# Kernel optimization log

Hardware: AMD Instinct MI355X
Metric: run time of the kernel (lower is better)

Reference implementation:

```python
import jax, jax.numpy as jnp
import numpy as np

B, H, S, D = 2, 16, 2048, 64


def setup_inputs() -> dict:
    key = jax.random.key(0)
    kq, kk, kv, km = jax.random.split(key, 4)
    q = jax.random.normal(kq, (B, H, S, D), dtype=jnp.float32)
    k = jax.random.normal(kk, (B, H, S, D), dtype=jnp.float32)
    v = jax.random.normal(kv, (B, H, S, D), dtype=jnp.float32)
    # True = attend, False = masked out (padding)
    attention_mask = jax.random.randint(km, (B, S), 0, 2).astype(jnp.bool_)
    return {"q": q, "k": k, "v": v, "attention_mask": attention_mask}


def reference(q, k, v, attention_mask):
    scale = q.shape[-1] ** -0.5
    # sim: [B, H, S, S]
    sim = jnp.einsum("bhid,bhjd->bhij", q, k) * scale
    neg = jnp.finfo(sim.dtype).min
    # mask [B, S] -> [B, 1, 1, S]; keep where mask is True
    sim = jnp.where(attention_mask[:, None, None, :], sim, neg)
    attn = jax.nn.softmax(sim, axis=-1)
    out = jnp.einsum("bhij,bhjd->bhid", attn, v)
    return out
```

## Files before the change

kernel.cpp:

```cpp
#include <hip/hip_runtime.h>
#include <hip/hip_fp16.h>

namespace {
constexpr int kB = 2, kH = 16, kS = 2048, kD = 64, kBH = kB * kH;
constexpr int BQ = 128, BKV = 64;
constexpr int NQT = kS / BQ;

typedef _Float16 f16x8 __attribute__((ext_vector_type(8)));
typedef _Float16 f16x4 __attribute__((ext_vector_type(4)));
typedef __fp16 fp16x2 __attribute__((ext_vector_type(2)));
typedef float f32x16 __attribute__((ext_vector_type(16)));
typedef float f32x4 __attribute__((ext_vector_type(4)));
typedef unsigned int u32;

constexpr float kQScale = 0.125f * 1.4426950408889634f;

__device__ __forceinline__ int paddr(int row, int col) {
  const int prow = row >> 1;
  return prow * 128 + ((((row & 1) << 6) | col) ^ ((prow & 15) << 3));
}

__device__ __forceinline__ u32 pkrtz(float a, float b) {
  union { fp16x2 h; u32 u; } c;
  c.h = __builtin_amdgcn_cvt_pkrtz(a, b);
  return c.u;
}

__global__ __launch_bounds__(256) void scan_kernel(const int* __restrict__ M,
                                                   int* __restrict__ Idx,
                                                   float* __restrict__ BiasC,
                                                   int* __restrict__ NTarr) {
  const int b = blockIdx.x;
  const int tid = threadIdx.x;
  __shared__ int part[256];
  __shared__ int nvs;
  int m[8], sum = 0;
#pragma unroll
  for (int i = 0; i < 8; ++i) {
    m[i] = M[b * kS + tid * 8 + i];
    sum += m[i] ? 1 : 0;
  }
  part[tid] = sum;
  __syncthreads();
  for (int off = 1; off < 256; off <<= 1) {
    int v = (tid >= off) ? part[tid - off] : 0;
    __syncthreads();
    part[tid] += v;
    __syncthreads();
  }
  int run = part[tid] - sum;
#pragma unroll
  for (int i = 0; i < 8; ++i)
    if (m[i]) Idx[b * kS + run++] = tid * 8 + i;
  if (tid == 255) nvs = part[255];
  __syncthreads();
  const int Nv = nvs;
  int NT = (Nv + 63) >> 6;
  if (NT == 0) NT = 1;
  const int pad = NT * 64;
  for (int j = Nv + tid; j < pad; j += 256) Idx[b * kS + j] = 0;
#pragma unroll
  for (int i = 0; i < 8; ++i) {
    const int j = tid * 8 + i;
    BiasC[b * kS + j] = (j < Nv) ? 0.f : -1e30f;
  }
  if (tid == 0) NTarr[b] = NT;
}

__global__ __launch_bounds__(256) void gather_k_kernel(
    const float* __restrict__ K, const int* __restrict__ Idx,
    const int* __restrict__ NTarr, _Float16* __restrict__ Kc) {
  const int e = blockIdx.x * 256 + threadIdx.x;
  const int bh = e >> 14;
  const int rem = e & 16383;
  const int j = rem >> 3;
  const int d0 = (rem & 7) << 3;
  const int b = bh >> 4;
  if (j >= NTarr[b] * 64) return;
  const int src = Idx[b * kS + j];
  const float* p = K + ((size_t)bh * kS + src) * kD + d0;
  float4 x = *(const float4*)p;
  float4 y = *(const float4*)(p + 4);
  f16x8 o;
  o[0] = (_Float16)x.x; o[1] = (_Float16)x.y; o[2] = (_Float16)x.z; o[3] = (_Float16)x.w;
  o[4] = (_Float16)y.x; o[5] = (_Float16)y.y; o[6] = (_Float16)y.z; o[7] = (_Float16)y.w;
  *(f16x8*)(Kc + ((size_t)bh * kS + j) * kD + d0) = o;
}

__global__ __launch_bounds__(256) void gather_vt_kernel(
    const float* __restrict__ V, const int* __restrict__ Idx,
    const int* __restrict__ NTarr, _Float16* __restrict__ Vtc) {
  __shared__ _Float16 Vl[64 * 68];
  __shared__ int ridx[64];
  const int tid = threadIdx.x;
  const int bh = blockIdx.x >> 5;
  const int jt = blockIdx.x & 31;
  const int b = bh >> 4;
  if (jt >= NTarr[b]) return;
  if (tid < 64) ridx[tid] = Idx[b * kS + jt * 64 + tid];
  __syncthreads();
  const float* vb = V + (size_t)bh * kS * kD;
#pragma unroll
  for (int i = 0; i < 4; ++i) {
    int off = (tid + 256 * i) * 4;
    int r = off >> 6, c = off & 63;
    float4 x = *(const float4*)(vb + (size_t)ridx[r] * kD + c);
    Vl[(c + 0) * 68 + r] = (_Float16)x.x;
    Vl[(c + 1) * 68 + r] = (_Float16)x.y;
    Vl[(c + 2) * 68 + r] = (_Float16)x.z;
    Vl[(c + 3) * 68 + r] = (_Float16)x.w;
  }
  __syncthreads();
  const int d = tid >> 2, c0 = (tid & 3) * 16;
  _Float16* op = Vtc + ((size_t)bh * kD + d) * kS + jt * 64 + c0;
#pragma unroll
  for (int j = 0; j < 4; ++j)
    *(f16x4*)(op + 4 * j) = *(const f16x4*)(Vl + d * 68 + c0 + 4 * j);
}

__global__ __launch_bounds__(256, 2) void fattn_c(
    const _Float16* __restrict__ Kc, const _Float16* __restrict__ Vtc,
    const float* __restrict__ Q, const float* __restrict__ BiasC,
    const int* __restrict__ NTarr, float* __restrict__ O) {
  __shared__ __align__(16) char smem[16384 + 16384 + 512];
  _Float16* Kl = (_Float16*)smem;
  _Float16* Vl = (_Float16*)(smem + 16384);
  float* mbl = (float*)(smem + 32768);
  float* Os = (float*)smem;

  const int tid = threadIdx.x;
  const int lane = tid & 63;
  const int w = tid >> 6;
  const int q = lane & 31;
  const int h = lane >> 5;

  const int bid = blockIdx.x;
  const int cpx = gridDim.x >> 3;
  const int sbid = (bid & 7) * cpx + (bid >> 3);
  const int bh = sbid >> 4;
  const int qt = sbid & 15;
  const int q0 = qt * BQ;
  const int b = bh >> 4;
  const int NT = NTarr[b];

  f16x8 qf[4];
  {
    const float* qp = Q + ((size_t)bh * kS + q0 + w * 32 + q) * kD;
#pragma unroll
    for (int dc = 0; dc < 4; ++dc) {
      const float* p = qp + dc * 16 + h * 8;
      float4 x = *(const float4*)p;
      float4 y = *(const float4*)(p + 4);
      f16x8 a;
      a[0] = (_Float16)(x.x * kQScale); a[1] = (_Float16)(x.y * kQScale);
      a[2] = (_Float16)(x.z * kQScale); a[3] = (_Float16)(x.w * kQScale);
      a[4] = (_Float16)(y.x * kQScale); a[5] = (_Float16)(y.y * kQScale);
      a[6] = (_Float16)(y.z * kQScale); a[7] = (_Float16)(y.w * kQScale);
      qf[dc] = a;
    }
  }

  f32x16 oa[2];
#pragma unroll
  for (int i = 0; i < 16; ++i) { oa[0][i] = 0.f; oa[1][i] = 0.f; }
  float m_run = -30.f, l_run = 0.f;

  const _Float16* kb = Kc + (size_t)bh * kS * kD;
  const _Float16* vb = Vtc + (size_t)bh * kD * kS;
  const float* mpc = BiasC + b * kS;

  const int sr = tid >> 2, sc = (tid & 3) * 16;
  const int a0 = paddr(sr, sc), a1 = paddr(sr, sc + 8);

  {
    f16x8 k0 = *(const f16x8*)(kb + (size_t)sr * kD + sc);
    f16x8 k1 = *(const f16x8*)(kb + (size_t)sr * kD + sc + 8);
    f16x8 v0 = *(const f16x8*)(vb + (size_t)sr * kS + sc);
    f16x8 v1 = *(const f16x8*)(vb + (size_t)sr * kS + sc + 8);
    *(f16x8*)(Kl + a0) = k0; *(f16x8*)(Kl + a1) = k1;
    *(f16x8*)(Vl + a0) = v0; *(f16x8*)(Vl + a1) = v1;
    if (tid < 64) mbl[tid] = mpc[tid];
  }
  __syncthreads();

  int cur = 0;
  for (int t = 0; t < NT; ++t) {
    const int t0 = t * BKV;
    const bool pf = (t + 1 < NT);
    f16x8 nk0, nk1, nv0, nv1;
    float nmv = 0.f;
    if (pf) {
      const int n0 = t0 + BKV;
      nk0 = *(const f16x8*)(kb + (size_t)(n0 + sr) * kD + sc);
      nk1 = *(const f16x8*)(kb + (size_t)(n0 + sr) * kD + sc + 8);
      nv0 = *(const f16x8*)(vb + (size_t)sr * kS + n0 + sc);
      nv1 = *(const f16x8*)(vb + (size_t)sr * kS + n0 + sc + 8);
      if (tid < 64) nmv = mpc[n0 + tid];
    }

    const _Float16* kd = Kl + cur * 4096;
    const _Float16* vd = Vl + cur * 4096;
    const float* mb = mbl + cur * 64;

    f32x16 s[2];
    __builtin_amdgcn_s_setprio(1);
#pragma unroll
    for (int mt = 0; mt < 2; ++mt) {
      f32x16 z;
#pragma unroll
      for (int g = 0; g < 4; ++g) {
        f32x4 mv = *(const f32x4*)(mb + mt * 32 + 8 * g + 4 * h);
        z[4 * g + 0] = mv[0]; z[4 * g + 1] = mv[1];
        z[4 * g + 2] = mv[2]; z[4 * g + 3] = mv[3];
      }
#pragma unroll
      for (int dc = 0; dc < 4; ++dc) {
        f16x8 kf = *(const f16x8*)(kd + paddr(mt * 32 + q, dc * 16 + h * 8));
        z = __builtin_amdgcn_mfma_f32_32x32x16_f16(kf, qf[dc], z, 0, 0, 0);
      }
      s[mt] = z;
    }
    __builtin_amdgcn_s_setprio(0);

    float mx = -3.0e38f;
#pragma unroll
    for (int mt = 0; mt < 2; ++mt)
#pragma unroll
      for (int r = 0; r < 16; r += 2)
        mx = fmaxf(fmaxf(mx, s[mt][r]), s[mt][r + 1]);
    mx = fmaxf(mx, __shfl_xor(mx, 32));

    if (__any(mx > m_run + 8.f)) {
      const float mnew = fmaxf(m_run, mx);
      const float corr = __builtin_amdgcn_exp2f(m_run - mnew);
      m_run = mnew;
      l_run *= corr;
#pragma unroll
      for (int mt = 0; mt < 2; ++mt)
#pragma unroll
        for (int r = 0; r < 16; ++r) oa[mt][r] *= corr;
    }
    const float negm = -m_run;

    float ts = 0.f;
#pragma unroll
    for (int mt = 0; mt < 2; ++mt)
#pragma unroll
      for (int r = 0; r < 16; ++r) {
        float p = __builtin_amdgcn_exp2f(s[mt][r] + negm);
        s[mt][r] = p;
        ts += p;
      }
    ts += __shfl_xor(ts, 32);
    l_run += ts;

    u32 pkA[2][4], pkB[2][4];
#pragma unroll
    for (int mt = 0; mt < 2; ++mt)
#pragma unroll
      for (int g = 0; g < 4; ++g) {
        pkA[mt][g] = pkrtz(s[mt][4 * g + 0], s[mt][4 * g + 1]);
        pkB[mt][g] = pkrtz(s[mt][4 * g + 2], s[mt][4 * g + 3]);
      }

    __builtin_amdgcn_s_setprio(1);
#pragma unroll
    for (int kk = 0; kk < 4; ++kk) {
      const int e = kk & 1, mt = kk >> 1;
      u32 crossA = __shfl_xor(h ? pkA[mt][2 * e] : pkA[mt][2 * e + 1], 32);
      u32 crossB = __shfl_xor(h ? pkB[mt][2 * e] : pkB[mt][2 * e + 1], 32);
      union { u32 u[4]; f16x8 v; } pb;
      pb.u[0] = h ? crossA : pkA[mt][2 * e];
      pb.u[1] = h ? crossB : pkB[mt][2 * e];
      pb.u[2] = h ? pkA[mt][2 * e + 1] : crossA;
      pb.u[3] = h ? pkB[mt][2 * e + 1] : crossB;
#pragma unroll
      for (int md = 0; md < 2; ++md) {
        f16x8 vf = *(const f16x8*)(vd + paddr(md * 32 + q, kk * 16 + h * 8));
        oa[md] = __builtin_amdgcn_mfma_f32_32x32x16_f16(vf, pb.v, oa[md], 0, 0, 0);
      }
    }
    __builtin_amdgcn_s_setprio(0);

    if (pf) {
      _Float16* kd2 = Kl + (cur ^ 1) * 4096;
      _Float16* vd2 = Vl + (cur ^ 1) * 4096;
      *(f16x8*)(kd2 + a0) = nk0; *(f16x8*)(kd2 + a1) = nk1;
      *(f16x8*)(vd2 + a0) = nv0; *(f16x8*)(vd2 + a1) = nv1;
      if (tid < 64) mbl[(cur ^ 1) * 64 + tid] = nmv;
    }
    __syncthreads();
    cur ^= 1;
  }

  const float inv = 1.f / l_run;
#pragma unroll
  for (int ph = 0; ph < 2; ++ph) {
    __syncthreads();
    if ((w >> 1) == ph) {
#pragma unroll
      for (int mt = 0; mt < 2; ++mt)
#pragma unroll
        for (int r = 0; r < 16; ++r) {
          int d = mt * 32 + (r & 3) + 8 * (r >> 2) + 4 * h;
          Os[((w & 1) * 32 + q) * 68 + d] = oa[mt][r] * inv;
        }
    }
    __syncthreads();
    {
      const int row = tid >> 2, cb = (tid & 3) * 16;
      float* op = O + ((size_t)bh * kS + q0 + ph * 64 + row) * kD + cb;
      const float* sp = Os + row * 68 + cb;
#pragma unroll
      for (int j = 0; j < 4; ++j) *(float4*)(op + 4 * j) = *(const float4*)(sp + 4 * j);
    }
  }
}

__device__ __forceinline__ int swz(int row, int colh) {
  return row * 64 + (colh ^ ((row & 7) << 3));
}

__global__ __launch_bounds__(256, 4) void fattn_fallback(
    const float* __restrict__ Q, const float* __restrict__ K,
    const float* __restrict__ V, const int* __restrict__ M,
    float* __restrict__ O) {
  __shared__ __align__(16) _Float16 Kl[64 * 64];
  __shared__ __align__(16) _Float16 Vtl[64 * 64];
  __shared__ __align__(16) _Float16 Pl[64 * 64];
  __shared__ float mbl[64];

  const int tid = threadIdx.x;
  const int lane = tid & 63;
  const int w = tid >> 6;
  const int lr = lane & 15;
  const int hg = lane >> 4;
  const int NQT1 = kS / 64;
  const int bh = blockIdx.x / NQT1;
  const int qt = blockIdx.x % NQT1;
  const int b = bh / kH;
  const int q0 = qt * 64;

  f16x8 aq[2];
  {
    const int row = q0 + w * 16 + lr;
    const float* qp = Q + ((size_t)bh * kS + row) * kD;
#pragma unroll
    for (int kf = 0; kf < 2; ++kf) {
      const float* p = qp + kf * 32 + hg * 8;
      float4 x = *(const float4*)(p);
      float4 y = *(const float4*)(p + 4);
      f16x8 a;
      a[0] = (_Float16)(x.x * 0.125f); a[1] = (_Float16)(x.y * 0.125f);
      a[2] = (_Float16)(x.z * 0.125f); a[3] = (_Float16)(x.w * 0.125f);
      a[4] = (_Float16)(y.x * 0.125f); a[5] = (_Float16)(y.y * 0.125f);
      a[6] = (_Float16)(y.z * 0.125f); a[7] = (_Float16)(y.w * 0.125f);
      aq[kf] = a;
    }
  }

  f32x4 oacc[4];
#pragma unroll
  for (int c = 0; c < 4; ++c) { oacc[c][0]=0.f; oacc[c][1]=0.f; oacc[c][2]=0.f; oacc[c][3]=0.f; }
  float m_run[4], l_run[4];
#pragma unroll
  for (int r = 0; r < 4; ++r) { m_run[r] = -1e30f; l_run[r] = 0.f; }

  const float* kb = K + (size_t)bh * kS * kD;
  const float* vb = V + (size_t)bh * kS * kD;
  const int* mbp = M + b * kS;

  for (int t0 = 0; t0 < kS; t0 += 64) {
    __syncthreads();
#pragma unroll
    for (int i = 0; i < 4; ++i) {
      const int off = (tid + 256 * i) * 4;
      const int row = off >> 6;
      const int col = off & 63;
      float4 kx = *(const float4*)(kb + (size_t)(t0 + row) * kD + col);
      f16x4 hk;
      hk[0] = (_Float16)kx.x; hk[1] = (_Float16)kx.y;
      hk[2] = (_Float16)kx.z; hk[3] = (_Float16)kx.w;
      *(f16x4*)(Kl + swz(row, col)) = hk;
      float4 vx = *(const float4*)(vb + (size_t)(t0 + row) * kD + col);
      Vtl[swz(col + 0, row)] = (_Float16)vx.x;
      Vtl[swz(col + 1, row)] = (_Float16)vx.y;
      Vtl[swz(col + 2, row)] = (_Float16)vx.z;
      Vtl[swz(col + 3, row)] = (_Float16)vx.w;
    }
    if (tid < 64) mbl[tid] = mbp[t0 + tid] ? 0.f : -1e30f;
    __syncthreads();

    f32x4 s[4];
#pragma unroll
    for (int c = 0; c < 4; ++c) {
      f32x4 z; z[0]=0.f; z[1]=0.f; z[2]=0.f; z[3]=0.f;
#pragma unroll
      for (int kf = 0; kf < 2; ++kf) {
        f16x8 bk = *(const f16x8*)(Kl + swz(c * 16 + lr, kf * 32 + hg * 8));
        z = __builtin_amdgcn_mfma_f32_16x16x32_f16(aq[kf], bk, z, 0, 0, 0);
      }
      const float mval = mbl[c * 16 + lr];
#pragma unroll
      for (int r = 0; r < 4; ++r) z[r] += mval;
      s[c] = z;
    }

    float tmax[4];
#pragma unroll
    for (int r = 0; r < 4; ++r)
      tmax[r] = fmaxf(fmaxf(s[0][r], s[1][r]), fmaxf(s[2][r], s[3][r]));
#pragma unroll
    for (int off = 1; off < 16; off <<= 1)
#pragma unroll
      for (int r = 0; r < 4; ++r) tmax[r] = fmaxf(tmax[r], __shfl_xor(tmax[r], off));

    float mnew[4], corr[4], tsum[4];
#pragma unroll
    for (int r = 0; r < 4; ++r) {
      mnew[r] = fmaxf(m_run[r], tmax[r]);
      corr[r] = __expf(m_run[r] - mnew[r]);
      m_run[r] = mnew[r];
      tsum[r] = 0.f;
    }
#pragma unroll
    for (int c = 0; c < 4; ++c)
#pragma unroll
      for (int r = 0; r < 4; ++r) {
        const float p = __expf(s[c][r] - mnew[r]);
        tsum[r] += p;
        Pl[swz(w * 16 + hg * 4 + r, c * 16 + lr)] = (_Float16)p;
      }
#pragma unroll
    for (int off = 1; off < 16; off <<= 1)
#pragma unroll
      for (int r = 0; r < 4; ++r) tsum[r] += __shfl_xor(tsum[r], off);
#pragma unroll
    for (int r = 0; r < 4; ++r) l_run[r] = l_run[r] * corr[r] + tsum[r];
#pragma unroll
    for (int c = 0; c < 4; ++c)
#pragma unroll
      for (int r = 0; r < 4; ++r) oacc[c][r] *= corr[r];

#pragma unroll
    for (int kf = 0; kf < 2; ++kf) {
      f16x8 pa = *(const f16x8*)(Pl + swz(w * 16 + lr, kf * 32 + hg * 8));
#pragma unroll
      for (int cd = 0; cd < 4; ++cd) {
        f16x8 vbf = *(const f16x8*)(Vtl + swz(cd * 16 + lr, kf * 32 + hg * 8));
        oacc[cd] = __builtin_amdgcn_mfma_f32_16x16x32_f16(pa, vbf, oacc[cd], 0, 0, 0);
      }
    }
  }

#pragma unroll
  for (int r = 0; r < 4; ++r) {
    const float inv = 1.f / l_run[r];
    const int row = q0 + w * 16 + hg * 4 + r;
    float* op = O + ((size_t)bh * kS + row) * kD;
#pragma unroll
    for (int cd = 0; cd < 4; ++cd) op[cd * 16 + lr] = oacc[cd][r] * inv;
  }
}
}

extern "C" void kernel_launch(void* const* d_in, const int* in_sizes, int n_in,
                              void* d_out, int out_size, void* d_ws, size_t ws_size,
                              hipStream_t stream) {
  (void)in_sizes; (void)n_in; (void)out_size;
  const float* q = (const float*)d_in[0];
  const float* k = (const float*)d_in[1];
  const float* v = (const float*)d_in[2];
  const int* m = (const int*)d_in[3];
  float* o = (float*)d_out;

  const size_t elems = (size_t)kBH * kS * kD;
  const size_t need = 2 * elems * sizeof(_Float16)
                    + (size_t)kB * kS * sizeof(int)
                    + (size_t)kB * kS * sizeof(float)
                    + 256;

  if (ws_size >= need) {
    _Float16* Kc = (_Float16*)d_ws;
    _Float16* Vtc = Kc + elems;
    int* Idx = (int*)(Vtc + elems);
    float* BiasC = (float*)(Idx + (size_t)kB * kS);
    int* NTarr = (int*)(BiasC + (size_t)kB * kS);
    hipLaunchKernelGGL(scan_kernel, dim3(kB), dim3(256), 0, stream, m, Idx, BiasC, NTarr);
    hipLaunchKernelGGL(gather_k_kernel, dim3((kBH * kS * 8) / 256), dim3(256), 0, stream,
                       k, Idx, NTarr, Kc);
    hipLaunchKernelGGL(gather_vt_kernel, dim3(kBH * (kS / 64)), dim3(256), 0, stream,
                       v, Idx, NTarr, Vtc);
    hipLaunchKernelGGL(fattn_c, dim3(kBH * NQT), dim3(256), 0, stream,
                       Kc, Vtc, q, BiasC, NTarr, o);
  } else {
    hipLaunchKernelGGL(fattn_fallback, dim3(kBH * (kS / 64)), dim3(256), 0, stream,
                       q, k, v, m, o);
  }
}
```

Measured before the change: 54.57 us.

## Load K/V fragments directly from global into registers, dropping LDS staging

The attention kernel no longer stages K and V tiles through double-buffered shared memory with block-wide barriers. Each wave now loads its MFMA operand fragments straight from global memory (L2-cached) into registers, prefetching the next K tile and ping-ponging two register buffers. The mask bias is read from global too. Row max and sum reductions become tree reductions to shorten dependency chains. This removes LDS traffic and __syncthreads per tile, at the cost of each of the four waves reading the same K/V from global/L2 again and higher register pressure.

```diff
diff --git a/kernel.cpp b/kernel.cpp
--- a/kernel.cpp
+++ b/kernel.cpp
@@ -14,11 +14,6 @@
 typedef unsigned int u32;
 
 constexpr float kQScale = 0.125f * 1.4426950408889634f;
-
-__device__ __forceinline__ int paddr(int row, int col) {
-  const int prow = row >> 1;
-  return prow * 128 + ((((row & 1) << 6) | col) ^ ((prow & 15) << 3));
-}
 
 __device__ __forceinline__ u32 pkrtz(float a, float b) {
   union { fp16x2 h; u32 u; } c;
@@ -118,15 +113,11 @@
     *(f16x4*)(op + 4 * j) = *(const f16x4*)(Vl + d * 68 + c0 + 4 * j);
 }
 
-__global__ __launch_bounds__(256, 2) void fattn_c(
+__global__ __launch_bounds__(256, 2) void fattn_d(
     const _Float16* __restrict__ Kc, const _Float16* __restrict__ Vtc,
     const float* __restrict__ Q, const float* __restrict__ BiasC,
     const int* __restrict__ NTarr, float* __restrict__ O) {
-  __shared__ __align__(16) char smem[16384 + 16384 + 512];
-  _Float16* Kl = (_Float16*)smem;
-  _Float16* Vl = (_Float16*)(smem + 16384);
-  float* mbl = (float*)(smem + 32768);
-  float* Os = (float*)smem;
+  __shared__ float Os[64 * 68];
 
   const int tid = threadIdx.x;
   const int lane = tid & 63;
@@ -169,39 +160,34 @@
   const _Float16* vb = Vtc + (size_t)bh * kD * kS;
   const float* mpc = BiasC + b * kS;
 
-  const int sr = tid >> 2, sc = (tid & 3) * 16;
-  const int a0 = paddr(sr, sc), a1 = paddr(sr, sc + 8);
-
-  {
-    f16x8 k0 = *(const f16x8*)(kb + (size_t)sr * kD + sc);
-    f16x8 k1 = *(const f16x8*)(kb + (size_t)sr * kD + sc + 8);
-    f16x8 v0 = *(const f16x8*)(vb + (size_t)sr * kS + sc);
-    f16x8 v1 = *(const f16x8*)(vb + (size_t)sr * kS + sc + 8);
-    *(f16x8*)(Kl + a0) = k0; *(f16x8*)(Kl + a1) = k1;
-    *(f16x8*)(Vl + a0) = v0; *(f16x8*)(Vl + a1) = v1;
-    if (tid < 64) mbl[tid] = mpc[tid];
-  }
-  __syncthreads();
-
-  int cur = 0;
-  for (int t = 0; t < NT; ++t) {
-    const int t0 = t * BKV;
-    const bool pf = (t + 1 < NT);
-    f16x8 nk0, nk1, nv0, nv1;
-    float nmv = 0.f;
-    if (pf) {
-      const int n0 = t0 + BKV;
-      nk0 = *(const f16x8*)(kb + (size_t)(n0 + sr) * kD + sc);
-      nk1 = *(const f16x8*)(kb + (size_t)(n0 + sr) * kD + sc + 8);
-      nv0 = *(const f16x8*)(vb + (size_t)sr * kS + n0 + sc);
-      nv1 = *(const f16x8*)(vb + (size_t)sr * kS + n0 + sc + 8);
-      if (tid < 64) nmv = mpc[n0 + tid];
-    }
-
-    const _Float16* kd = Kl + cur * 4096;
-    const _Float16* vd = Vl + cur * 4096;
-    const float* mb = mbl + cur * 64;
-
+  const _Float16* kbase0 = kb + (q + 0) * 64 + h * 8;
+  const _Float16* kbase1 = kb + (q + 32) * 64 + h * 8;
+  const _Float16* vbase0 = vb + (size_t)(q + 0) * kS + h * 8;
+  const _Float16* vbase1 = vb + (size_t)(q + 32) * kS + h * 8;
+
+  f16x8 kA[8], kB[8], vr[8];
+  auto loadK = [&](int t, f16x8 (&kr)[8]) {
+    const int off = t * 4096;
+#pragma unroll
+    for (int dc = 0; dc < 4; ++dc) {
+      kr[dc] = *(const f16x8*)(kbase0 + off + dc * 16);
+      kr[4 + dc] = *(const f16x8*)(kbase1 + off + dc * 16);
+    }
+  };
+  auto loadV = [&](int t) {
+    const int off = t * 64;
+#pragma unroll
+    for (int kk = 0; kk < 4; ++kk) {
+      vr[kk] = *(const f16x8*)(vbase0 + off + kk * 16);
+      vr[4 + kk] = *(const f16x8*)(vbase1 + off + kk * 16);
+    }
+  };
+
+  auto body = [&](int t, f16x8 (&kcur)[8], f16x8 (&knext)[8], bool pf) {
+    loadV(t);
+    if (pf) loadK(t + 1, knext);
+
+    const float* mb = mpc + t * 64;
     f32x16 s[2];
     __builtin_amdgcn_s_setprio(1);
 #pragma unroll
@@ -214,21 +200,20 @@
         z[4 * g + 2] = mv[2]; z[4 * g + 3] = mv[3];
       }
 #pragma unroll
-      for (int dc = 0; dc < 4; ++dc) {
-        f16x8 kf = *(const f16x8*)(kd + paddr(mt * 32 + q, dc * 16 + h * 8));
-        z = __builtin_amdgcn_mfma_f32_32x32x16_f16(kf, qf[dc], z, 0, 0, 0);
-      }
+      for (int dc = 0; dc < 4; ++dc)
+        z = __builtin_amdgcn_mfma_f32_32x32x16_f16(kcur[mt * 4 + dc], qf[dc], z, 0, 0, 0);
       s[mt] = z;
     }
     __builtin_amdgcn_s_setprio(0);
 
-    float mx = -3.0e38f;
-#pragma unroll
-    for (int mt = 0; mt < 2; ++mt)
-#pragma unroll
-      for (int r = 0; r < 16; r += 2)
-        mx = fmaxf(fmaxf(mx, s[mt][r]), s[mt][r + 1]);
-    mx = fmaxf(mx, __shfl_xor(mx, 32));
+    float tm[16];
+#pragma unroll
+    for (int i = 0; i < 16; ++i) tm[i] = fmaxf(s[0][i], s[1][i]);
+#pragma unroll
+    for (int st = 8; st > 0; st >>= 1)
+#pragma unroll
+      for (int i = 0; i < st; ++i) tm[i] = fmaxf(tm[i], tm[i + st]);
+    const float mx = fmaxf(tm[0], __shfl_xor(tm[0], 32));
 
     if (__any(mx > m_run + 8.f)) {
       const float mnew = fmaxf(m_run, mx);
@@ -242,56 +227,55 @@
     }
     const float negm = -m_run;
 
-    float ts = 0.f;
 #pragma unroll
     for (int mt = 0; mt < 2; ++mt)
 #pragma unroll
-      for (int r = 0; r < 16; ++r) {
-        float p = __builtin_amdgcn_exp2f(s[mt][r] + negm);
-        s[mt][r] = p;
-        ts += p;
-      }
-    ts += __shfl_xor(ts, 32);
-    l_run += ts;
-
-    u32 pkA[2][4], pkB[2][4];
+      for (int r = 0; r < 16; ++r)
+        s[mt][r] = __builtin_amdgcn_exp2f(s[mt][r] + negm);
+    float tsum[16];
+#pragma unroll
+    for (int i = 0; i < 16; ++i) tsum[i] = s[0][i] + s[1][i];
+#pragma unroll
+    for (int st = 8; st > 0; st >>= 1)
+#pragma unroll
+      for (int i = 0; i < st; ++i) tsum[i] += tsum[i + st];
+    l_run += tsum[0] + __shfl_xor(tsum[0], 32);
+
+    u32 pkA_[2][4], pkB_[2][4];
 #pragma unroll
     for (int mt = 0; mt < 2; ++mt)
 #pragma unroll
       for (int g = 0; g < 4; ++g) {
-        pkA[mt][g] = pkrtz(s[mt][4 * g + 0], s[mt][4 * g + 1]);
-        pkB[mt][g] = pkrtz(s[mt][4 * g + 2], s[mt][4 * g + 3]);
+        pkA_[mt][g] = pkrtz(s[mt][4 * g + 0], s[mt][4 * g + 1]);
+        pkB_[mt][g] = pkrtz(s[mt][4 * g + 2], s[mt][4 * g + 3]);
       }
 
     __builtin_amdgcn_s_setprio(1);
 #pragma unroll
     for (int kk = 0; kk < 4; ++kk) {
       const int e = kk & 1, mt = kk >> 1;
-      u32 crossA = __shfl_xor(h ? pkA[mt][2 * e] : pkA[mt][2 * e + 1], 32);
-      u32 crossB = __shfl_xor(h ? pkB[mt][2 * e] : pkB[mt][2 * e + 1], 32);
+      u32 crossA = __shfl_xor(h ? pkA_[mt][2 * e] : pkA_[mt][2 * e + 1], 32);
+      u32 crossB = __shfl_xor(h ? pkB_[mt][2 * e] : pkB_[mt][2 * e + 1], 32);
       union { u32 u[4]; f16x8 v; } pb;
-      pb.u[0] = h ? crossA : pkA[mt][2 * e];
-      pb.u[1] = h ? crossB : pkB[mt][2 * e];
-      pb.u[2] = h ? pkA[mt][2 * e + 1] : crossA;
-      pb.u[3] = h ? pkB[mt][2 * e + 1] : crossB;
-#pragma unroll
-      for (int md = 0; md < 2; ++md) {
-        f16x8 vf = *(const f16x8*)(vd + paddr(md * 32 + q, kk * 16 + h * 8));
-        oa[md] = __builtin_amdgcn_mfma_f32_32x32x16_f16(vf, pb.v, oa[md], 0, 0, 0);
-      }
+      pb.u[0] = h ? crossA : pkA_[mt][2 * e];
+      pb.u[1] = h ? crossB : pkB_[mt][2 * e];
+      pb.u[2] = h ? pkA_[mt][2 * e + 1] : crossA;
+      pb.u[3] = h ? pkB_[mt][2 * e + 1] : crossB;
+#pragma unroll
+      for (int md = 0; md < 2; ++md)
+        oa[md] = __builtin_amdgcn_mfma_f32_32x32x16_f16(vr[md * 4 + kk], pb.v, oa[md], 0, 0, 0);
     }
     __builtin_amdgcn_s_setprio(0);
-
-    if (pf) {
-      _Float16* kd2 = Kl + (cur ^ 1) * 4096;
-      _Float16* vd2 = Vl + (cur ^ 1) * 4096;
-      *(f16x8*)(kd2 + a0) = nk0; *(f16x8*)(kd2 + a1) = nk1;
-      *(f16x8*)(vd2 + a0) = nv0; *(f16x8*)(vd2 + a1) = nv1;
-      if (tid < 64) mbl[(cur ^ 1) * 64 + tid] = nmv;
-    }
-    __syncthreads();
-    cur ^= 1;
-  }
+  };
+
+  loadK(0, kA);
+  int t = 0;
+  while (t + 2 <= NT) {
+    body(t, kA, kB, true);
+    body(t + 1, kB, kA, t + 2 < NT);
+    t += 2;
+  }
+  if (t < NT) body(t, kA, kB, false);
 
   const float inv = 1.f / l_run;
 #pragma unroll
@@ -491,7 +475,7 @@
                        k, Idx, NTarr, Kc);
     hipLaunchKernelGGL(gather_vt_kernel, dim3(kBH * (kS / 64)), dim3(256), 0, stream,
                        v, Idx, NTarr, Vtc);
-    hipLaunchKernelGGL(fattn_c, dim3(kBH * NQT), dim3(256), 0, stream,
+    hipLaunchKernelGGL(fattn_d, dim3(kBH * NQT), dim3(256), 0, stream,
                        Kc, Vtc, q, BiasC, NTarr, o);
   } else {
     hipLaunchKernelGGL(fattn_fallback, dim3(kBH * (kS / 64)), dim3(256), 0, stream,
```

After: 97.26 us. 78.2% more time.

## Split KV range across two wavegroups per block with in-block softmax merge

Applied to the files above, without the earlier changes.

Halves the query tile to 64 rows and doubles the grid. Each block's two 128-thread halves now process separate halves of the compacted KV tiles, each with its own double-buffered LDS, and their partial (m, l, O) states are merged through shared memory at the end. NT is padded to an even count so the split is balanced. The max and sum reductions are also rewritten as trees to shorten the dependency chains. The goal is more parallelism and shorter per-block serial KV loops, at the cost of 65KB of LDS per block (which may limit occupancy), a merge epilogue, and K/V being reloaded by twice as many blocks.

```diff
diff --git a/kernel.cpp b/kernel.cpp
--- a/kernel.cpp
+++ b/kernel.cpp
@@ -3,7 +3,7 @@
 
 namespace {
 constexpr int kB = 2, kH = 16, kS = 2048, kD = 64, kBH = kB * kH;
-constexpr int BQ = 128, BKV = 64;
+constexpr int BQ = 64, BKV = 64;
 constexpr int NQT = kS / BQ;
 
 typedef _Float16 f16x8 __attribute__((ext_vector_type(8)));
@@ -57,6 +57,7 @@
   const int Nv = nvs;
   int NT = (Nv + 63) >> 6;
   if (NT == 0) NT = 1;
+  NT += (NT & 1);
   const int pad = NT * 64;
   for (int j = Nv + tid; j < pad; j += 256) Idx[b * kS + j] = 0;
 #pragma unroll
@@ -118,34 +119,37 @@
     *(f16x4*)(op + 4 * j) = *(const f16x4*)(Vl + d * 68 + c0 + 4 * j);
 }
 
-__global__ __launch_bounds__(256, 2) void fattn_c(
+__global__ __launch_bounds__(256, 2) void fattn_m(
     const _Float16* __restrict__ Kc, const _Float16* __restrict__ Vtc,
     const float* __restrict__ Q, const float* __restrict__ BiasC,
     const int* __restrict__ NTarr, float* __restrict__ O) {
-  __shared__ __align__(16) char smem[16384 + 16384 + 512];
-  _Float16* Kl = (_Float16*)smem;
-  _Float16* Vl = (_Float16*)(smem + 16384);
-  float* mbl = (float*)(smem + 32768);
-  float* Os = (float*)smem;
+  __shared__ __align__(16) char smem[66560];
 
   const int tid = threadIdx.x;
   const int lane = tid & 63;
-  const int w = tid >> 6;
   const int q = lane & 31;
   const int h = lane >> 5;
+  const int pr = tid >> 7;
+  const int pw = (tid >> 6) & 1;
 
   const int bid = blockIdx.x;
   const int cpx = gridDim.x >> 3;
   const int sbid = (bid & 7) * cpx + (bid >> 3);
-  const int bh = sbid >> 4;
-  const int qt = sbid & 15;
+  const int bh = sbid >> 5;
+  const int qt = sbid & 31;
   const int q0 = qt * BQ;
   const int b = bh >> 4;
   const int NT = NTarr[b];
+  const int NTh = NT >> 1;
+  const int g0 = pr * NTh;
+
+  _Float16* Kl = (_Float16*)(smem + pr * 32768);
+  _Float16* Vl = (_Float16*)(smem + pr * 32768 + 16384);
+  float* mbl = (float*)(smem + 65536 + pr * 512);
 
   f16x8 qf[4];
   {
-    const float* qp = Q + ((size_t)bh * kS + q0 + w * 32 + q) * kD;
+    const float* qp = Q + ((size_t)bh * kS + q0 + pw * 32 + q) * kD;
 #pragma unroll
     for (int dc = 0; dc < 4; ++dc) {
       const float* p = qp + dc * 16 + h * 8;
@@ -169,34 +173,43 @@
   const _Float16* vb = Vtc + (size_t)bh * kD * kS;
   const float* mpc = BiasC + b * kS;
 
-  const int sr = tid >> 2, sc = (tid & 3) * 16;
-  const int a0 = paddr(sr, sc), a1 = paddr(sr, sc + 8);
-
-  {
-    f16x8 k0 = *(const f16x8*)(kb + (size_t)sr * kD + sc);
-    f16x8 k1 = *(const f16x8*)(kb + (size_t)sr * kD + sc + 8);
-    f16x8 v0 = *(const f16x8*)(vb + (size_t)sr * kS + sc);
-    f16x8 v1 = *(const f16x8*)(vb + (size_t)sr * kS + sc + 8);
-    *(f16x8*)(Kl + a0) = k0; *(f16x8*)(Kl + a1) = k1;
-    *(f16x8*)(Vl + a0) = v0; *(f16x8*)(Vl + a1) = v1;
-    if (tid < 64) mbl[tid] = mpc[tid];
-  }
+  const int ptid = tid & 127;
+  const int sr = ptid >> 1, scb = (ptid & 1) * 32;
+  int adr[4];
+#pragma unroll
+  for (int c = 0; c < 4; ++c) adr[c] = paddr(sr, scb + 8 * c);
+
+  f16x8 nk[4], nv[4];
+  float nmb = 0.f;
+  auto loadT = [&](int g) {
+    const _Float16* kp = kb + (size_t)(g * 64 + sr) * kD + scb;
+    const _Float16* vp = vb + (size_t)sr * kS + g * 64 + scb;
+#pragma unroll
+    for (int c = 0; c < 4; ++c) {
+      nk[c] = *(const f16x8*)(kp + 8 * c);
+      nv[c] = *(const f16x8*)(vp + 8 * c);
+    }
+    if (ptid < 64) nmb = mpc[g * 64 + ptid];
+  };
+  auto writeT = [&](int buf) {
+    _Float16* kd = Kl + buf * 4096;
+    _Float16* vd = Vl + buf * 4096;
+#pragma unroll
+    for (int c = 0; c < 4; ++c) {
+      *(f16x8*)(kd + adr[c]) = nk[c];
+      *(f16x8*)(vd + adr[c]) = nv[c];
+    }
+    if (ptid < 64) mbl[buf * 64 + ptid] = nmb;
+  };
+
+  loadT(g0);
+  writeT(0);
   __syncthreads();
 
   int cur = 0;
-  for (int t = 0; t < NT; ++t) {
-    const int t0 = t * BKV;
-    const bool pf = (t + 1 < NT);
-    f16x8 nk0, nk1, nv0, nv1;
-    float nmv = 0.f;
-    if (pf) {
-      const int n0 = t0 + BKV;
-      nk0 = *(const f16x8*)(kb + (size_t)(n0 + sr) * kD + sc);
-      nk1 = *(const f16x8*)(kb + (size_t)(n0 + sr) * kD + sc + 8);
-      nv0 = *(const f16x8*)(vb + (size_t)sr * kS + n0 + sc);
-      nv1 = *(const f16x8*)(vb + (size_t)sr * kS + n0 + sc + 8);
-      if (tid < 64) nmv = mpc[n0 + tid];
-    }
+  for (int i = 0; i < NTh; ++i) {
+    const bool pf = (i + 1 < NTh);
+    if (pf) loadT(g0 + i + 1);
 
     const _Float16* kd = Kl + cur * 4096;
     const _Float16* vd = Vl + cur * 4096;
@@ -222,13 +235,14 @@
     }
     __builtin_amdgcn_s_setprio(0);
 
-    float mx = -3.0e38f;
-#pragma unroll
-    for (int mt = 0; mt < 2; ++mt)
-#pragma unroll
-      for (int r = 0; r < 16; r += 2)
-        mx = fmaxf(fmaxf(mx, s[mt][r]), s[mt][r + 1]);
-    mx = fmaxf(mx, __shfl_xor(mx, 32));
+    float tm[16];
+#pragma unroll
+    for (int i2 = 0; i2 < 16; ++i2) tm[i2] = fmaxf(s[0][i2], s[1][i2]);
+#pragma unroll
+    for (int st = 8; st > 0; st >>= 1)
+#pragma unroll
+      for (int i2 = 0; i2 < st; ++i2) tm[i2] = fmaxf(tm[i2], tm[i2 + st]);
+    const float mx = fmaxf(tm[0], __shfl_xor(tm[0], 32));
 
     if (__any(mx > m_run + 8.f)) {
       const float mnew = fmaxf(m_run, mx);
@@ -242,17 +256,19 @@
     }
     const float negm = -m_run;
 
-    float ts = 0.f;
 #pragma unroll
     for (int mt = 0; mt < 2; ++mt)
 #pragma unroll
-      for (int r = 0; r < 16; ++r) {
-        float p = __builtin_amdgcn_exp2f(s[mt][r] + negm);
-        s[mt][r] = p;
-        ts += p;
-      }
-    ts += __shfl_xor(ts, 32);
-    l_run += ts;
+      for (int r = 0; r < 16; ++r)
+        s[mt][r] = __builtin_amdgcn_exp2f(s[mt][r] + negm);
+    float tsum[16];
+#pragma unroll
+    for (int i2 = 0; i2 < 16; ++i2) tsum[i2] = s[0][i2] + s[1][i2];
+#pragma unroll
+    for (int st = 8; st > 0; st >>= 1)
+#pragma unroll
+      for (int i2 = 0; i2 < st; ++i2) tsum[i2] += tsum[i2 + st];
+    l_run += tsum[0] + __shfl_xor(tsum[0], 32);
 
     u32 pkA[2][4], pkB[2][4];
 #pragma unroll
@@ -282,38 +298,46 @@
     }
     __builtin_amdgcn_s_setprio(0);
 
-    if (pf) {
-      _Float16* kd2 = Kl + (cur ^ 1) * 4096;
-      _Float16* vd2 = Vl + (cur ^ 1) * 4096;
-      *(f16x8*)(kd2 + a0) = nk0; *(f16x8*)(kd2 + a1) = nk1;
-      *(f16x8*)(vd2 + a0) = nv0; *(f16x8*)(vd2 + a1) = nv1;
-      if (tid < 64) mbl[(cur ^ 1) * 64 + tid] = nmv;
-    }
+    if (pf) writeT(cur ^ 1);
     __syncthreads();
     cur ^= 1;
   }
 
-  const float inv = 1.f / l_run;
-#pragma unroll
-  for (int ph = 0; ph < 2; ++ph) {
-    __syncthreads();
-    if ((w >> 1) == ph) {
-#pragma unroll
-      for (int mt = 0; mt < 2; ++mt)
-#pragma unroll
-        for (int r = 0; r < 16; ++r) {
-          int d = mt * 32 + (r & 3) + 8 * (r >> 2) + 4 * h;
-          Os[((w & 1) * 32 + q) * 68 + d] = oa[mt][r] * inv;
-        }
-    }
-    __syncthreads();
-    {
-      const int row = tid >> 2, cb = (tid & 3) * 16;
-      float* op = O + ((size_t)bh * kS + q0 + ph * 64 + row) * kD + cb;
-      const float* sp = Os + row * 68 + cb;
-#pragma unroll
-      for (int j = 0; j < 4; ++j) *(float4*)(op + 4 * j) = *(const float4*)(sp + 4 * j);
-    }
+  float* O1 = (float*)(smem + 32768);
+  float* ml1 = (float*)(smem + 49152);
+  if (pr == 1) {
+#pragma unroll
+    for (int mt = 0; mt < 2; ++mt)
+#pragma unroll
+      for (int r = 0; r < 16; ++r)
+        O1[(mt * 16 + r) * 128 + (pw * 32 + q) * 2 + h] = oa[mt][r];
+    if (h == 0) *(float2*)(ml1 + (pw * 32 + q) * 2) = make_float2(m_run, l_run);
+  }
+  __syncthreads();
+  float* Os = (float*)smem;
+  if (pr == 0) {
+    const float2 m1l1 = *(const float2*)(ml1 + (pw * 32 + q) * 2);
+    const float mm = fmaxf(m_run, m1l1.x);
+    float w0 = __builtin_amdgcn_exp2f(m_run - mm);
+    float w1 = __builtin_amdgcn_exp2f(m1l1.x - mm);
+    const float inv = 1.f / (l_run * w0 + m1l1.y * w1);
+    w0 *= inv; w1 *= inv;
+#pragma unroll
+    for (int mt = 0; mt < 2; ++mt)
+#pragma unroll
+      for (int r = 0; r < 16; ++r) {
+        const int d = mt * 32 + (r & 3) + 8 * (r >> 2) + 4 * h;
+        const float v1 = O1[(mt * 16 + r) * 128 + (pw * 32 + q) * 2 + h];
+        Os[(pw * 32 + q) * 68 + d] = oa[mt][r] * w0 + v1 * w1;
+      }
+  }
+  __syncthreads();
+  {
+    const int row = tid >> 2, cb = (tid & 3) * 16;
+    float* op = O + ((size_t)bh * kS + q0 + row) * kD + cb;
+    const float* sp = Os + row * 68 + cb;
+#pragma unroll
+    for (int j = 0; j < 4; ++j) *(float4*)(op + 4 * j) = *(const float4*)(sp + 4 * j);
   }
 }
 
@@ -491,7 +515,7 @@
                        k, Idx, NTarr, Kc);
     hipLaunchKernelGGL(gather_vt_kernel, dim3(kBH * (kS / 64)), dim3(256), 0, stream,
                        v, Idx, NTarr, Vtc);
-    hipLaunchKernelGGL(fattn_c, dim3(kBH * NQT), dim3(256), 0, stream,
+    hipLaunchKernelGGL(fattn_m, dim3(kBH * NQT), dim3(256), 0, stream,
                        Kc, Vtc, q, BiasC, NTarr, o);
   } else {
     hipLaunchKernelGGL(fattn_fallback, dim3(kBH * (kS / 64)), dim3(256), 0, stream,
```

After: 63.05 us. +15.5%, slower.

## Fuse K and V gather kernels and replace bias buffer with tail masking

Applied to the files above, without the earlier changes.

Merges the separate K-gather and V-transpose-gather kernels into one launch that shares the loaded row indices, dropping one kernel launch. Removes the per-key bias array: the attention kernel now starts MFMA accumulators at zero and masks only the padded keys of the final tile by comparing against the valid-key count. Max and sum reductions become tree reductions to shorten dependency chains. This trades LDS bias loads and stores per tile for a branch on the last tile.

```diff
diff --git a/kernel.cpp b/kernel.cpp
--- a/kernel.cpp
+++ b/kernel.cpp
@@ -28,8 +28,8 @@
 
 __global__ __launch_bounds__(256) void scan_kernel(const int* __restrict__ M,
                                                    int* __restrict__ Idx,
-                                                   float* __restrict__ BiasC,
-                                                   int* __restrict__ NTarr) {
+                                                   int* __restrict__ NTarr,
+                                                   int* __restrict__ Nvarr) {
   const int b = blockIdx.x;
   const int tid = threadIdx.x;
   __shared__ int part[256];
@@ -59,37 +59,13 @@
   if (NT == 0) NT = 1;
   const int pad = NT * 64;
   for (int j = Nv + tid; j < pad; j += 256) Idx[b * kS + j] = 0;
-#pragma unroll
-  for (int i = 0; i < 8; ++i) {
-    const int j = tid * 8 + i;
-    BiasC[b * kS + j] = (j < Nv) ? 0.f : -1e30f;
-  }
-  if (tid == 0) NTarr[b] = NT;
-}
-
-__global__ __launch_bounds__(256) void gather_k_kernel(
-    const float* __restrict__ K, const int* __restrict__ Idx,
-    const int* __restrict__ NTarr, _Float16* __restrict__ Kc) {
-  const int e = blockIdx.x * 256 + threadIdx.x;
-  const int bh = e >> 14;
-  const int rem = e & 16383;
-  const int j = rem >> 3;
-  const int d0 = (rem & 7) << 3;
-  const int b = bh >> 4;
-  if (j >= NTarr[b] * 64) return;
-  const int src = Idx[b * kS + j];
-  const float* p = K + ((size_t)bh * kS + src) * kD + d0;
-  float4 x = *(const float4*)p;
-  float4 y = *(const float4*)(p + 4);
-  f16x8 o;
-  o[0] = (_Float16)x.x; o[1] = (_Float16)x.y; o[2] = (_Float16)x.z; o[3] = (_Float16)x.w;
-  o[4] = (_Float16)y.x; o[5] = (_Float16)y.y; o[6] = (_Float16)y.z; o[7] = (_Float16)y.w;
-  *(f16x8*)(Kc + ((size_t)bh * kS + j) * kD + d0) = o;
-}
-
-__global__ __launch_bounds__(256) void gather_vt_kernel(
-    const float* __restrict__ V, const int* __restrict__ Idx,
-    const int* __restrict__ NTarr, _Float16* __restrict__ Vtc) {
+  if (tid == 0) { NTarr[b] = NT; Nvarr[b] = Nv; }
+}
+
+__global__ __launch_bounds__(256) void gather_kv_kernel(
+    const float* __restrict__ K, const float* __restrict__ V,
+    const int* __restrict__ Idx, const int* __restrict__ NTarr,
+    _Float16* __restrict__ Kc, _Float16* __restrict__ Vtc) {
   __shared__ _Float16 Vl[64 * 68];
   __shared__ int ridx[64];
   const int tid = threadIdx.x;
@@ -99,6 +75,22 @@
   if (jt >= NTarr[b]) return;
   if (tid < 64) ridx[tid] = Idx[b * kS + jt * 64 + tid];
   __syncthreads();
+
+  const float* kbase = K + (size_t)bh * kS * kD;
+  _Float16* kout = Kc + ((size_t)bh * kS + jt * 64) * kD;
+#pragma unroll
+  for (int it = 0; it < 2; ++it) {
+    const int e = tid + 256 * it;
+    const int row = e >> 3, d0 = (e & 7) * 8;
+    const float* p = kbase + (size_t)ridx[row] * kD + d0;
+    float4 x = *(const float4*)p;
+    float4 y = *(const float4*)(p + 4);
+    f16x8 o;
+    o[0] = (_Float16)x.x; o[1] = (_Float16)x.y; o[2] = (_Float16)x.z; o[3] = (_Float16)x.w;
+    o[4] = (_Float16)y.x; o[5] = (_Float16)y.y; o[6] = (_Float16)y.z; o[7] = (_Float16)y.w;
+    *(f16x8*)(kout + (size_t)row * kD + d0) = o;
+  }
+
   const float* vb = V + (size_t)bh * kS * kD;
 #pragma unroll
   for (int i = 0; i < 4; ++i) {
@@ -120,12 +112,11 @@
 
 __global__ __launch_bounds__(256, 2) void fattn_c(
     const _Float16* __restrict__ Kc, const _Float16* __restrict__ Vtc,
-    const float* __restrict__ Q, const float* __restrict__ BiasC,
-    const int* __restrict__ NTarr, float* __restrict__ O) {
-  __shared__ __align__(16) char smem[16384 + 16384 + 512];
+    const float* __restrict__ Q, const int* __restrict__ NTarr,
+    const int* __restrict__ Nvarr, float* __restrict__ O) {
+  __shared__ __align__(16) char smem[32768];
   _Float16* Kl = (_Float16*)smem;
   _Float16* Vl = (_Float16*)(smem + 16384);
-  float* mbl = (float*)(smem + 32768);
   float* Os = (float*)smem;
 
   const int tid = threadIdx.x;
@@ -142,6 +133,7 @@
   const int q0 = qt * BQ;
   const int b = bh >> 4;
   const int NT = NTarr[b];
+  const int Nv = Nvarr[b];
 
   f16x8 qf[4];
   {
@@ -163,11 +155,13 @@
   f32x16 oa[2];
 #pragma unroll
   for (int i = 0; i < 16; ++i) { oa[0][i] = 0.f; oa[1][i] = 0.f; }
+  f32x16 kZero;
+#pragma unroll
+  for (int i = 0; i < 16; ++i) kZero[i] = 0.f;
   float m_run = -30.f, l_run = 0.f;
 
   const _Float16* kb = Kc + (size_t)bh * kS * kD;
   const _Float16* vb = Vtc + (size_t)bh * kD * kS;
-  const float* mpc = BiasC + b * kS;
 
   const int sr = tid >> 2, sc = (tid & 3) * 16;
   const int a0 = paddr(sr, sc), a1 = paddr(sr, sc + 8);
@@ -179,7 +173,6 @@
     f16x8 v1 = *(const f16x8*)(vb + (size_t)sr * kS + sc + 8);
     *(f16x8*)(Kl + a0) = k0; *(f16x8*)(Kl + a1) = k1;
     *(f16x8*)(Vl + a0) = v0; *(f16x8*)(Vl + a1) = v1;
-    if (tid < 64) mbl[tid] = mpc[tid];
   }
   __syncthreads();
 
@@ -188,31 +181,22 @@
     const int t0 = t * BKV;
     const bool pf = (t + 1 < NT);
     f16x8 nk0, nk1, nv0, nv1;
-    float nmv = 0.f;
     if (pf) {
       const int n0 = t0 + BKV;
       nk0 = *(const f16x8*)(kb + (size_t)(n0 + sr) * kD + sc);
       nk1 = *(const f16x8*)(kb + (size_t)(n0 + sr) * kD + sc + 8);
       nv0 = *(const f16x8*)(vb + (size_t)sr * kS + n0 + sc);
       nv1 = *(const f16x8*)(vb + (size_t)sr * kS + n0 + sc + 8);
-      if (tid < 64) nmv = mpc[n0 + tid];
     }
 
     const _Float16* kd = Kl + cur * 4096;
     const _Float16* vd = Vl + cur * 4096;
-    const float* mb = mbl + cur * 64;
 
     f32x16 s[2];
     __builtin_amdgcn_s_setprio(1);
 #pragma unroll
     for (int mt = 0; mt < 2; ++mt) {
-      f32x16 z;
-#pragma unroll
-      for (int g = 0; g < 4; ++g) {
-        f32x4 mv = *(const f32x4*)(mb + mt * 32 + 8 * g + 4 * h);
-        z[4 * g + 0] = mv[0]; z[4 * g + 1] = mv[1];
-        z[4 * g + 2] = mv[2]; z[4 * g + 3] = mv[3];
-      }
+      f32x16 z = kZero;
 #pragma unroll
       for (int dc = 0; dc < 4; ++dc) {
         f16x8 kf = *(const f16x8*)(kd + paddr(mt * 32 + q, dc * 16 + h * 8));
@@ -222,13 +206,25 @@
     }
     __builtin_amdgcn_s_setprio(0);
 
-    float mx = -3.0e38f;
-#pragma unroll
-    for (int mt = 0; mt < 2; ++mt)
-#pragma unroll
-      for (int r = 0; r < 16; r += 2)
-        mx = fmaxf(fmaxf(mx, s[mt][r]), s[mt][r + 1]);
-    mx = fmaxf(mx, __shfl_xor(mx, 32));
+    if (t == NT - 1) {
+      const int kbase = t0 + 4 * h;
+#pragma unroll
+      for (int mt = 0; mt < 2; ++mt)
+#pragma unroll
+        for (int r = 0; r < 16; ++r) {
+          const int key = kbase + mt * 32 + 8 * (r >> 2) + (r & 3);
+          if (key >= Nv) s[mt][r] = -1e30f;
+        }
+    }
+
+    float tm[16];
+#pragma unroll
+    for (int i = 0; i < 16; ++i) tm[i] = fmaxf(s[0][i], s[1][i]);
+#pragma unroll
+    for (int st = 8; st > 0; st >>= 1)
+#pragma unroll
+      for (int i = 0; i < st; ++i) tm[i] = fmaxf(tm[i], tm[i + st]);
+    const float mx = fmaxf(tm[0], __shfl_xor(tm[0], 32));
 
     if (__any(mx > m_run + 8.f)) {
       const float mnew = fmaxf(m_run, mx);
@@ -242,17 +238,19 @@
     }
     const float negm = -m_run;
 
-    float ts = 0.f;
 #pragma unroll
     for (int mt = 0; mt < 2; ++mt)
 #pragma unroll
-      for (int r = 0; r < 16; ++r) {
-        float p = __builtin_amdgcn_exp2f(s[mt][r] + negm);
-        s[mt][r] = p;
-        ts += p;
-      }
-    ts += __shfl_xor(ts, 32);
-    l_run += ts;
+      for (int r = 0; r < 16; ++r)
+        s[mt][r] = __builtin_amdgcn_exp2f(s[mt][r] + negm);
+    float tsum[16];
+#pragma unroll
+    for (int i = 0; i < 16; ++i) tsum[i] = s[0][i] + s[1][i];
+#pragma unroll
+    for (int st = 8; st > 0; st >>= 1)
+#pragma unroll
+      for (int i = 0; i < st; ++i) tsum[i] += tsum[i + st];
+    l_run += tsum[0] + __shfl_xor(tsum[0], 32);
 
     u32 pkA[2][4], pkB[2][4];
 #pragma unroll
@@ -287,7 +285,6 @@
       _Float16* vd2 = Vl + (cur ^ 1) * 4096;
       *(f16x8*)(kd2 + a0) = nk0; *(f16x8*)(kd2 + a1) = nk1;
       *(f16x8*)(vd2 + a0) = nv0; *(f16x8*)(vd2 + a1) = nv1;
-      if (tid < 64) mbl[(cur ^ 1) * 64 + tid] = nmv;
     }
     __syncthreads();
     cur ^= 1;
@@ -477,22 +474,19 @@
   const size_t elems = (size_t)kBH * kS * kD;
   const size_t need = 2 * elems * sizeof(_Float16)
                     + (size_t)kB * kS * sizeof(int)
-                    + (size_t)kB * kS * sizeof(float)
-                    + 256;
+                    + 512;
 
   if (ws_size >= need) {
     _Float16* Kc = (_Float16*)d_ws;
     _Float16* Vtc = Kc + elems;
     int* Idx = (int*)(Vtc + elems);
-    float* BiasC = (float*)(Idx + (size_t)kB * kS);
-    int* NTarr = (int*)(BiasC + (size_t)kB * kS);
-    hipLaunchKernelGGL(scan_kernel, dim3(kB), dim3(256), 0, stream, m, Idx, BiasC, NTarr);
-    hipLaunchKernelGGL(gather_k_kernel, dim3((kBH * kS * 8) / 256), dim3(256), 0, stream,
-                       k, Idx, NTarr, Kc);
-    hipLaunchKernelGGL(gather_vt_kernel, dim3(kBH * (kS / 64)), dim3(256), 0, stream,
-                       v, Idx, NTarr, Vtc);
+    int* NTarr = Idx + (size_t)kB * kS;
+    int* Nvarr = NTarr + 64;
+    hipLaunchKernelGGL(scan_kernel, dim3(kB), dim3(256), 0, stream, m, Idx, NTarr, Nvarr);
+    hipLaunchKernelGGL(gather_kv_kernel, dim3(kBH * (kS / 64)), dim3(256), 0, stream,
+                       k, v, Idx, NTarr, Kc, Vtc);
     hipLaunchKernelGGL(fattn_c, dim3(kBH * NQT), dim3(256), 0, stream,
-                       Kc, Vtc, q, BiasC, NTarr, o);
+                       Kc, Vtc, q, NTarr, Nvarr, o);
   } else {
     hipLaunchKernelGGL(fattn_fallback, dim3(kBH * (kS / 64)), dim3(256), 0, stream,
                        q, k, v, m, o);
```

New measurement: 52.35 us. 4.1% less time.
